# Kernel tuning notes

Hardware: AMD Instinct MI355X
Metric: run time of the kernel (lower is better)

## Reference

```python
import jax, jax.numpy as jnp
import numpy as np

B, T, D = 64, 2048, 256


def setup_inputs() -> dict:
    key = jax.random.key(0)
    k_x, k_len, k_w, k_b, k_a = jax.random.split(key, 5)
    xs = jax.random.normal(k_x, (B, T, D), dtype=jnp.float32)
    # ragged lengths -> prefix mask, mimicking per-sample slicing in the torch loop
    lens = jax.random.randint(k_len, (B,), T // 4, T + 1)
    mask = (jnp.arange(T)[None, :] < lens[:, None]).astype(jnp.int32)
    mask2 = jnp.ones((B, T), dtype=jnp.int32)  # unused by the module
    W = jax.random.normal(k_w, (D, D), dtype=jnp.float32) * (1.0 / np.sqrt(D))
    b = jax.random.normal(k_b, (D,), dtype=jnp.float32) * 0.01
    attn = jax.random.normal(k_a, (D,), dtype=jnp.float32)  # nn.Parameter(D,1) squeezed
    return {"xs": xs, "mask": mask, "mask2": mask2, "W": W, "b": b, "attn": attn}


def reference(xs, mask, mask2, W, b, attn):
    # h = tanh(Linear(x)); torch Linear: x @ W.T + b
    h = jnp.tanh(jnp.einsum("btd,ed->bte", xs, W) + b)          # [B,T,D]
    scores = jnp.einsum("btd,d->bt", h, attn)                    # [B,T]
    valid = mask.astype(bool)
    scores = jnp.where(valid, scores, -jnp.inf)                  # softmax over valid frames only
    w = jax.nn.softmax(scores, axis=1)[..., None]                # [B,T,1]
    mu = jnp.sum(xs * w, axis=1)                                 # [B,D]
    var = jnp.maximum(jnp.sum(xs * xs * w, axis=1) - mu * mu, 1e-5)
    return jnp.concatenate([mu, jnp.sqrt(var)], axis=1)          # [B,2D]
```

## Files before the change

kernel.cpp:

```cpp
#include <hip/hip_runtime.h>
#include <hip/hip_bf16.h>
#include <math.h>

#define PB 64
#define PT 2048
#define PD 256
#define PM (PB * PT)
#define SBM 64
#define NT (PM / SBM)
#define TPB (PT / SBM)

typedef __bf16 bf16x8 __attribute__((ext_vector_type(8)));
typedef short  s16x8  __attribute__((ext_vector_type(8)));
typedef float  f32x4  __attribute__((ext_vector_type(4)));

__device__ __forceinline__ short rne_bf16(float x) {
    unsigned u = __builtin_bit_cast(unsigned, x);
    return (short)((u + 0x7fffu + ((u >> 16) & 1u)) >> 16);
}

__device__ __forceinline__ void split_bf16(float x, short& hi, short& lo) {
    unsigned u = __builtin_bit_cast(unsigned, x);
    hi = (short)(u >> 16);
    float hf = __builtin_bit_cast(float, u & 0xffff0000u);
    lo = rne_bf16(x - hf);
}

__global__ __launch_bounds__(256) void prep_kernel(
    const float* __restrict__ W, short* __restrict__ Whi, short* __restrict__ Wlo)
{
    const int idx = blockIdx.x * 256 + threadIdx.x;
    const int e = idx >> 8;
    const int k = idx & 255;
    short h, l;
    split_bf16(W[idx], h, l);
    const int flat = (((e >> 4) * 8 + (k >> 5)) * 64 + ((k & 31) >> 3) * 16 + (e & 15)) * 8 + (k & 7);
    Whi[flat] = h;
    Wlo[flat] = l;
}

__global__ __launch_bounds__(256, 4) void score_kernel(
    const float* __restrict__ xs, const short* __restrict__ Whi,
    const short* __restrict__ Wlo, const float* __restrict__ bias,
    const float* __restrict__ attn, const int* __restrict__ mask,
    float* __restrict__ stats, float* __restrict__ part)
{
    __shared__ __align__(16) short Ah[4 * 8 * 64 * 8];
    __shared__ float sred[4][64];
    __shared__ float lw[64];

    const int tid  = threadIdx.x;
    const int tile = blockIdx.x;
    const int bm   = tile * SBM;

    const int mv = mask[bm + (tid & 63)];
    if (__ballot(mv != 0) == 0ull) {
        if (tid == 0) { stats[tile * 2] = -INFINITY; stats[tile * 2 + 1] = 0.f; }
        return;
    }

#pragma unroll
    for (int p = 0; p < 8; ++p) {
        const int r  = p * 8 + (tid >> 5);
        const int kb = tid & 31;
        const float4 a0 = *(const float4*)&xs[(bm + r) * PD + kb * 8];
        const float4 a1 = *(const float4*)&xs[(bm + r) * PD + kb * 8 + 4];
        const float f[8] = {a0.x, a0.y, a0.z, a0.w, a1.x, a1.y, a1.z, a1.w};
        s16x8 h;
#pragma unroll
        for (int j = 0; j < 8; ++j) h[j] = rne_bf16(f[j]);
        const int mt = r >> 4, m_loc = r & 15;
        const int kt = kb >> 2, quad = kb & 3;
        const int msw = m_loc ^ (kb & 7);
        *(s16x8*)&Ah[(((mt * 8 + kt) * 64) + quad * 16 + msw) * 8] = h;
    }
    __syncthreads();

    const int lane = tid & 63;
    const int w    = tid >> 6;
    const int quad = lane >> 4;
    const int nl   = lane & 15;

    f32x4 acc[4][4] = {};

#pragma unroll 2
    for (int kt = 0; kt < 8; ++kt) {
        bf16x8 bh[4], bl[4];
#pragma unroll
        for (int n = 0; n < 4; ++n) {
            const int nt = w * 4 + n;
            const int bidx = ((nt * 8 + kt) * 64 + lane) * 8;
            bh[n] = *(const bf16x8*)&Whi[bidx];
            bl[n] = *(const bf16x8*)&Wlo[bidx];
        }
        s16x8 ah[4];
        const int msw = nl ^ ((kt * 4 + quad) & 7);
#pragma unroll
        for (int m = 0; m < 4; ++m)
            ah[m] = *(const s16x8*)&Ah[((m * 8 + kt) * 64 + quad * 16 + msw) * 8];
#pragma unroll
        for (int m = 0; m < 4; ++m) {
            const bf16x8 ahm = __builtin_bit_cast(bf16x8, ah[m]);
#pragma unroll
            for (int n = 0; n < 4; ++n) {
                acc[m][n] = __builtin_amdgcn_mfma_f32_16x16x32_bf16(ahm, bh[n], acc[m][n], 0, 0, 0);
                acc[m][n] = __builtin_amdgcn_mfma_f32_16x16x32_bf16(ahm, bl[n], acc[m][n], 0, 0, 0);
            }
        }
    }

    float bv[4], av[4];
#pragma unroll
    for (int n = 0; n < 4; ++n) {
        const int col = w * 64 + n * 16 + nl;
        bv[n] = bias[col];
        av[n] = attn[col];
    }
#pragma unroll
    for (int m = 0; m < 4; ++m) {
        float rs[4] = {0.f, 0.f, 0.f, 0.f};
#pragma unroll
        for (int n = 0; n < 4; ++n) {
#pragma unroll
            for (int r = 0; r < 4; ++r) {
                const float u  = acc[m][n][r] + bv[n];
                const float e2 = __expf(2.f * u);
                const float th = 1.f - 2.f * __builtin_amdgcn_rcpf(e2 + 1.f);
                rs[r] = fmaf(th, av[n], rs[r]);
            }
        }
#pragma unroll
        for (int off = 1; off < 16; off <<= 1) {
#pragma unroll
            for (int r = 0; r < 4; ++r) rs[r] += __shfl_xor(rs[r], off);
        }
        if (nl == 0) {
#pragma unroll
            for (int r = 0; r < 4; ++r) sred[w][m * 16 + quad * 4 + r] = rs[r];
        }
    }
    __syncthreads();

    if (tid < 64) {
        float s = sred[0][tid] + sred[1][tid] + sred[2][tid] + sred[3][tid];
        const bool vld = (mv != 0);
        s = vld ? s : -INFINITY;
        float mx = s;
#pragma unroll
        for (int off = 1; off < 64; off <<= 1) mx = fmaxf(mx, __shfl_xor(mx, off));
        const float wt = vld ? __expf(s - mx) : 0.f;
        float zs = wt;
#pragma unroll
        for (int off = 1; off < 64; off <<= 1) zs += __shfl_xor(zs, off);
        lw[tid] = wt;
        if (tid == 0) { stats[tile * 2] = mx; stats[tile * 2 + 1] = zs; }
    }
    __syncthreads();

    float4* rmu = (float4*)Ah;
    float4* rm2 = rmu + 4 * 64;
    const int c  = tid & 63;
    const int tq = tid >> 6;
    float4 mu = {0.f, 0.f, 0.f, 0.f};
    float4 m2 = {0.f, 0.f, 0.f, 0.f};
#pragma unroll
    for (int i = 0; i < 16; ++i) {
        const int r  = tq * 16 + i;
        const float wv = lw[r];
        const float4 x = *(const float4*)&xs[(bm + r) * PD + c * 4];
        mu.x = fmaf(wv, x.x, mu.x); mu.y = fmaf(wv, x.y, mu.y);
        mu.z = fmaf(wv, x.z, mu.z); mu.w = fmaf(wv, x.w, mu.w);
        m2.x = fmaf(wv * x.x, x.x, m2.x); m2.y = fmaf(wv * x.y, x.y, m2.y);
        m2.z = fmaf(wv * x.z, x.z, m2.z); m2.w = fmaf(wv * x.w, x.w, m2.w);
    }
    rmu[tq * 64 + c] = mu;
    rm2[tq * 64 + c] = m2;
    __syncthreads();

    if (tid < 64) {
        float4 smu = rmu[tid], sm2 = rm2[tid];
#pragma unroll
        for (int q = 1; q < 4; ++q) {
            const float4 a = rmu[q * 64 + tid], d = rm2[q * 64 + tid];
            smu.x += a.x; smu.y += a.y; smu.z += a.z; smu.w += a.w;
            sm2.x += d.x; sm2.y += d.y; sm2.z += d.z; sm2.w += d.w;
        }
        const int base = tile * 512;
        *(float4*)&part[base + tid * 4]       = smu;
        *(float4*)&part[base + 256 + tid * 4] = sm2;
    }
}

__global__ __launch_bounds__(256) void finalize_kernel(
    const float* __restrict__ stats, const float* __restrict__ part,
    float* __restrict__ out)
{
    const int b = blockIdx.x;
    const int d = threadIdx.x;

    float M = -INFINITY;
#pragma unroll
    for (int t = 0; t < TPB; ++t) M = fmaxf(M, stats[(b * TPB + t) * 2]);

    float Z = 0.f, m1 = 0.f, m2 = 0.f;
#pragma unroll 4
    for (int t = 0; t < TPB; ++t) {
        const int g = b * TPB + t;
        const float zt = stats[g * 2 + 1];
        if (zt > 0.f) {
            const float f = __expf(stats[g * 2] - M);
            Z  = fmaf(zt, f, Z);
            m1 = fmaf(part[g * 512 + d],       f, m1);
            m2 = fmaf(part[g * 512 + 256 + d], f, m2);
        }
    }
    const float inv = 1.f / Z;
    m1 *= inv;
    m2 *= inv;
    const float var = fmaxf(m2 - m1 * m1, 1e-5f);
    out[b * 512 + d]       = m1;
    out[b * 512 + 256 + d] = sqrtf(var);
}

extern "C" void kernel_launch(void* const* d_in, const int* in_sizes, int n_in,
                              void* d_out, int out_size, void* d_ws, size_t ws_size,
                              hipStream_t stream) {
    const float* xs   = (const float*)d_in[0];
    const int*   mask = (const int*)d_in[1];
    const float* W    = (const float*)d_in[3];
    const float* bias = (const float*)d_in[4];
    const float* attn = (const float*)d_in[5];
    float* out = (float*)d_out;

    float* stats = (float*)d_ws;
    float* part  = stats + NT * 2;
    short* Whi   = (short*)(part + NT * 512);
    short* Wlo   = Whi + PD * PD;

    prep_kernel<<<PD * PD / 256, 256, 0, stream>>>(W, Whi, Wlo);
    score_kernel<<<NT, 256, 0, stream>>>(xs, Whi, Wlo, bias, attn, mask, stats, part);
    finalize_kernel<<<PB, 256, 0, stream>>>(stats, part, out);
}
```

Baseline: 229.2 us.

## Make score kernel persistent with W fragments held in registers across tiles

The score kernel becomes persistent: 256 blocks of 512 threads each process 8 tiles. Each wave loads its slice of the hi/lo bf16 W fragments into registers once and reuses them for every tile, instead of reloading W per k-step in every one of 2048 blocks. Tiles are interleaved so each block's tiles come from different batches, which spreads the work from masked-out tiles. The cost is heavy register pressure (32 bf16x8 vectors per thread), fewer blocks, and extra syncs inside the loop, which may limit latency hiding.

```diff
diff --git a/kernel.cpp b/kernel.cpp
--- a/kernel.cpp
+++ b/kernel.cpp
@@ -7,7 +7,7 @@
 #define PD 256
 #define PM (PB * PT)
 #define SBM 64
-#define NT (PM / SBM)
+#define NTILES (PM / SBM)
 #define TPB (PT / SBM)
 
 typedef __bf16 bf16x8 __attribute__((ext_vector_type(8)));
@@ -39,155 +39,162 @@
     Wlo[flat] = l;
 }
 
-__global__ __launch_bounds__(256, 4) void score_kernel(
+__global__ __launch_bounds__(512, 2) void score_kernel(
     const float* __restrict__ xs, const short* __restrict__ Whi,
     const short* __restrict__ Wlo, const float* __restrict__ bias,
     const float* __restrict__ attn, const int* __restrict__ mask,
     float* __restrict__ stats, float* __restrict__ part)
 {
     __shared__ __align__(16) short Ah[4 * 8 * 64 * 8];
-    __shared__ float sred[4][64];
+    __shared__ float sred[8][64];
     __shared__ float lw[64];
 
     const int tid  = threadIdx.x;
-    const int tile = blockIdx.x;
-    const int bm   = tile * SBM;
-
-    const int mv = mask[bm + (tid & 63)];
-    if (__ballot(mv != 0) == 0ull) {
-        if (tid == 0) { stats[tile * 2] = -INFINITY; stats[tile * 2 + 1] = 0.f; }
-        return;
-    }
-
-#pragma unroll
-    for (int p = 0; p < 8; ++p) {
-        const int r  = p * 8 + (tid >> 5);
-        const int kb = tid & 31;
-        const float4 a0 = *(const float4*)&xs[(bm + r) * PD + kb * 8];
-        const float4 a1 = *(const float4*)&xs[(bm + r) * PD + kb * 8 + 4];
-        const float f[8] = {a0.x, a0.y, a0.z, a0.w, a1.x, a1.y, a1.z, a1.w};
-        s16x8 h;
-#pragma unroll
-        for (int j = 0; j < 8; ++j) h[j] = rne_bf16(f[j]);
-        const int mt = r >> 4, m_loc = r & 15;
-        const int kt = kb >> 2, quad = kb & 3;
-        const int msw = m_loc ^ (kb & 7);
-        *(s16x8*)&Ah[(((mt * 8 + kt) * 64) + quad * 16 + msw) * 8] = h;
-    }
-    __syncthreads();
-
     const int lane = tid & 63;
     const int w    = tid >> 6;
     const int quad = lane >> 4;
     const int nl   = lane & 15;
-
-    f32x4 acc[4][4] = {};
-
-#pragma unroll 2
-    for (int kt = 0; kt < 8; ++kt) {
-        bf16x8 bh[4], bl[4];
-#pragma unroll
-        for (int n = 0; n < 4; ++n) {
-            const int nt = w * 4 + n;
+    const int blk  = blockIdx.x;
+
+    bf16x8 Bh[2][8], Bl[2][8];
+#pragma unroll
+    for (int n = 0; n < 2; ++n) {
+#pragma unroll
+        for (int kt = 0; kt < 8; ++kt) {
+            const int nt   = w * 2 + n;
             const int bidx = ((nt * 8 + kt) * 64 + lane) * 8;
-            bh[n] = *(const bf16x8*)&Whi[bidx];
-            bl[n] = *(const bf16x8*)&Wlo[bidx];
-        }
-        s16x8 ah[4];
-        const int msw = nl ^ ((kt * 4 + quad) & 7);
-#pragma unroll
-        for (int m = 0; m < 4; ++m)
-            ah[m] = *(const s16x8*)&Ah[((m * 8 + kt) * 64 + quad * 16 + msw) * 8];
-#pragma unroll
-        for (int m = 0; m < 4; ++m) {
-            const bf16x8 ahm = __builtin_bit_cast(bf16x8, ah[m]);
-#pragma unroll
-            for (int n = 0; n < 4; ++n) {
-                acc[m][n] = __builtin_amdgcn_mfma_f32_16x16x32_bf16(ahm, bh[n], acc[m][n], 0, 0, 0);
-                acc[m][n] = __builtin_amdgcn_mfma_f32_16x16x32_bf16(ahm, bl[n], acc[m][n], 0, 0, 0);
-            }
-        }
-    }
-
-    float bv[4], av[4];
-#pragma unroll
-    for (int n = 0; n < 4; ++n) {
-        const int col = w * 64 + n * 16 + nl;
+            Bh[n][kt] = *(const bf16x8*)&Whi[bidx];
+            Bl[n][kt] = *(const bf16x8*)&Wlo[bidx];
+        }
+    }
+    float bv[2], av[2];
+#pragma unroll
+    for (int n = 0; n < 2; ++n) {
+        const int col = w * 32 + n * 16 + nl;
         bv[n] = bias[col];
         av[n] = attn[col];
     }
-#pragma unroll
-    for (int m = 0; m < 4; ++m) {
-        float rs[4] = {0.f, 0.f, 0.f, 0.f};
-#pragma unroll
-        for (int n = 0; n < 4; ++n) {
-#pragma unroll
-            for (int r = 0; r < 4; ++r) {
-                const float u  = acc[m][n][r] + bv[n];
-                const float e2 = __expf(2.f * u);
-                const float th = 1.f - 2.f * __builtin_amdgcn_rcpf(e2 + 1.f);
-                rs[r] = fmaf(th, av[n], rs[r]);
-            }
-        }
-#pragma unroll
-        for (int off = 1; off < 16; off <<= 1) {
-#pragma unroll
-            for (int r = 0; r < 4; ++r) rs[r] += __shfl_xor(rs[r], off);
-        }
-        if (nl == 0) {
-#pragma unroll
-            for (int r = 0; r < 4; ++r) sred[w][m * 16 + quad * 4 + r] = rs[r];
-        }
-    }
-    __syncthreads();
-
-    if (tid < 64) {
-        float s = sred[0][tid] + sred[1][tid] + sred[2][tid] + sred[3][tid];
-        const bool vld = (mv != 0);
-        s = vld ? s : -INFINITY;
-        float mx = s;
-#pragma unroll
-        for (int off = 1; off < 64; off <<= 1) mx = fmaxf(mx, __shfl_xor(mx, off));
-        const float wt = vld ? __expf(s - mx) : 0.f;
-        float zs = wt;
-#pragma unroll
-        for (int off = 1; off < 64; off <<= 1) zs += __shfl_xor(zs, off);
-        lw[tid] = wt;
-        if (tid == 0) { stats[tile * 2] = mx; stats[tile * 2 + 1] = zs; }
-    }
-    __syncthreads();
-
-    float4* rmu = (float4*)Ah;
-    float4* rm2 = rmu + 4 * 64;
-    const int c  = tid & 63;
-    const int tq = tid >> 6;
-    float4 mu = {0.f, 0.f, 0.f, 0.f};
-    float4 m2 = {0.f, 0.f, 0.f, 0.f};
-#pragma unroll
-    for (int i = 0; i < 16; ++i) {
-        const int r  = tq * 16 + i;
-        const float wv = lw[r];
-        const float4 x = *(const float4*)&xs[(bm + r) * PD + c * 4];
-        mu.x = fmaf(wv, x.x, mu.x); mu.y = fmaf(wv, x.y, mu.y);
-        mu.z = fmaf(wv, x.z, mu.z); mu.w = fmaf(wv, x.w, mu.w);
-        m2.x = fmaf(wv * x.x, x.x, m2.x); m2.y = fmaf(wv * x.y, x.y, m2.y);
-        m2.z = fmaf(wv * x.z, x.z, m2.z); m2.w = fmaf(wv * x.w, x.w, m2.w);
-    }
-    rmu[tq * 64 + c] = mu;
-    rm2[tq * 64 + c] = m2;
-    __syncthreads();
-
-    if (tid < 64) {
-        float4 smu = rmu[tid], sm2 = rm2[tid];
-#pragma unroll
-        for (int q = 1; q < 4; ++q) {
-            const float4 a = rmu[q * 64 + tid], d = rm2[q * 64 + tid];
-            smu.x += a.x; smu.y += a.y; smu.z += a.z; smu.w += a.w;
-            sm2.x += d.x; sm2.y += d.y; sm2.z += d.z; sm2.w += d.w;
-        }
-        const int base = tile * 512;
-        *(float4*)&part[base + tid * 4]       = smu;
-        *(float4*)&part[base + 256 + tid * 4] = sm2;
+
+    for (int i = 0; i < 8; ++i) {
+        const int tile = (blk & 63) * 32 + i * 4 + (blk >> 6);
+        const int bm   = tile * SBM;
+
+        const int mv = mask[bm + lane];
+        if (__ballot(mv != 0) == 0ull) {
+            if (tid == 0) { stats[tile * 2] = -INFINITY; stats[tile * 2 + 1] = 0.f; }
+            continue;
+        }
+
+        __syncthreads();
+
+#pragma unroll
+        for (int p = 0; p < 4; ++p) {
+            const int r  = p * 16 + (tid >> 5);
+            const int kb = tid & 31;
+            const float4 a0 = *(const float4*)&xs[(bm + r) * PD + kb * 8];
+            const float4 a1 = *(const float4*)&xs[(bm + r) * PD + kb * 8 + 4];
+            const float f[8] = {a0.x, a0.y, a0.z, a0.w, a1.x, a1.y, a1.z, a1.w};
+            s16x8 h;
+#pragma unroll
+            for (int j = 0; j < 8; ++j) h[j] = rne_bf16(f[j]);
+            const int mt = r >> 4, m_loc = r & 15;
+            const int kt = kb >> 2, qd = kb & 3;
+            const int msw = m_loc ^ (kb & 7);
+            *(s16x8*)&Ah[(((mt * 8 + kt) * 64) + qd * 16 + msw) * 8] = h;
+        }
+        __syncthreads();
+
+        f32x4 acc[4][2] = {};
+#pragma unroll
+        for (int kt = 0; kt < 8; ++kt) {
+            s16x8 ah[4];
+            const int msw = nl ^ ((kt * 4 + quad) & 7);
+#pragma unroll
+            for (int m = 0; m < 4; ++m)
+                ah[m] = *(const s16x8*)&Ah[((m * 8 + kt) * 64 + quad * 16 + msw) * 8];
+#pragma unroll
+            for (int m = 0; m < 4; ++m) {
+                const bf16x8 ahm = __builtin_bit_cast(bf16x8, ah[m]);
+#pragma unroll
+                for (int n = 0; n < 2; ++n) {
+                    acc[m][n] = __builtin_amdgcn_mfma_f32_16x16x32_bf16(ahm, Bh[n][kt], acc[m][n], 0, 0, 0);
+                    acc[m][n] = __builtin_amdgcn_mfma_f32_16x16x32_bf16(ahm, Bl[n][kt], acc[m][n], 0, 0, 0);
+                }
+            }
+        }
+
+#pragma unroll
+        for (int m = 0; m < 4; ++m) {
+            float rs[4] = {0.f, 0.f, 0.f, 0.f};
+#pragma unroll
+            for (int n = 0; n < 2; ++n) {
+#pragma unroll
+                for (int r = 0; r < 4; ++r) {
+                    const float u  = acc[m][n][r] + bv[n];
+                    const float e2 = __expf(2.f * u);
+                    const float th = 1.f - 2.f * __builtin_amdgcn_rcpf(e2 + 1.f);
+                    rs[r] = fmaf(th, av[n], rs[r]);
+                }
+            }
+#pragma unroll
+            for (int off = 1; off < 16; off <<= 1) {
+#pragma unroll
+                for (int r = 0; r < 4; ++r) rs[r] += __shfl_xor(rs[r], off);
+            }
+            if (nl == 0) {
+#pragma unroll
+                for (int r = 0; r < 4; ++r) sred[w][m * 16 + quad * 4 + r] = rs[r];
+            }
+        }
+        __syncthreads();
+
+        if (tid < 64) {
+            float s = sred[0][tid] + sred[1][tid] + sred[2][tid] + sred[3][tid]
+                    + sred[4][tid] + sred[5][tid] + sred[6][tid] + sred[7][tid];
+            const bool vld = (mv != 0);
+            s = vld ? s : -INFINITY;
+            float mx = s;
+#pragma unroll
+            for (int off = 1; off < 64; off <<= 1) mx = fmaxf(mx, __shfl_xor(mx, off));
+            const float wt = vld ? __expf(s - mx) : 0.f;
+            float zs = wt;
+#pragma unroll
+            for (int off = 1; off < 64; off <<= 1) zs += __shfl_xor(zs, off);
+            lw[tid] = wt;
+            if (tid == 0) { stats[tile * 2] = mx; stats[tile * 2 + 1] = zs; }
+        }
+        __syncthreads();
+
+        float4* rmu = (float4*)Ah;
+        float4* rm2 = rmu + 8 * 64;
+        float4 mu = {0.f, 0.f, 0.f, 0.f};
+        float4 m2 = {0.f, 0.f, 0.f, 0.f};
+#pragma unroll
+        for (int j = 0; j < 8; ++j) {
+            const int r  = w * 8 + j;
+            const float wv = lw[r];
+            const float4 x = *(const float4*)&xs[(bm + r) * PD + lane * 4];
+            mu.x = fmaf(wv, x.x, mu.x); mu.y = fmaf(wv, x.y, mu.y);
+            mu.z = fmaf(wv, x.z, mu.z); mu.w = fmaf(wv, x.w, mu.w);
+            m2.x = fmaf(wv * x.x, x.x, m2.x); m2.y = fmaf(wv * x.y, x.y, m2.y);
+            m2.z = fmaf(wv * x.z, x.z, m2.z); m2.w = fmaf(wv * x.w, x.w, m2.w);
+        }
+        rmu[w * 64 + lane] = mu;
+        rm2[w * 64 + lane] = m2;
+        __syncthreads();
+
+        if (tid < 64) {
+            float4 smu = rmu[tid], sm2 = rm2[tid];
+#pragma unroll
+            for (int q = 1; q < 8; ++q) {
+                const float4 a = rmu[q * 64 + tid], d = rm2[q * 64 + tid];
+                smu.x += a.x; smu.y += a.y; smu.z += a.z; smu.w += a.w;
+                sm2.x += d.x; sm2.y += d.y; sm2.z += d.z; sm2.w += d.w;
+            }
+            const int base = tile * 512;
+            *(float4*)&part[base + tid * 4]       = smu;
+            *(float4*)&part[base + 256 + tid * 4] = sm2;
+        }
     }
 }
 
@@ -233,11 +240,11 @@
     float* out = (float*)d_out;
 
     float* stats = (float*)d_ws;
-    float* part  = stats + NT * 2;
-    short* Whi   = (short*)(part + NT * 512);
+    float* part  = stats + NTILES * 2;
+    short* Whi   = (short*)(part + NTILES * 512);
     short* Wlo   = Whi + PD * PD;
 
     prep_kernel<<<PD * PD / 256, 256, 0, stream>>>(W, Whi, Wlo);
-    score_kernel<<<NT, 256, 0, stream>>>(xs, Whi, Wlo, bias, attn, mask, stats, part);
+    score_kernel<<<256, 512, 0, stream>>>(xs, Whi, Wlo, bias, attn, mask, stats, part);
     finalize_kernel<<<PB, 256, 0, stream>>>(stats, part, out);
 }
```

Result: slower. 242.0 us (+5.6%).

## Load A fragments directly from global, drop LDS staging and a barrier

Applied to the files above, without the earlier changes.

The score kernel no longer stages the bf16-converted x tile in shared memory. Each wave now reads its MFMA A fragments straight from global memory inside the k-loop and converts them with packed v_cvt_pk_bf16_f32. The softmax reduction now runs redundantly in every wave, and the weights are broadcast with __shfl instead of through LDS, which removes a __syncthreads and the lw buffer. The cost is that all four waves re-read the same x rows from global/L2 (four times the A traffic), and conversion now uses hardware rounding instead of the explicit RNE routine.

```diff
diff --git a/kernel.cpp b/kernel.cpp
--- a/kernel.cpp
+++ b/kernel.cpp
@@ -7,7 +7,7 @@
 #define PD 256
 #define PM (PB * PT)
 #define SBM 64
-#define NT (PM / SBM)
+#define NTILES (PM / SBM)
 #define TPB (PT / SBM)
 
 typedef __bf16 bf16x8 __attribute__((ext_vector_type(8)));
@@ -24,6 +24,12 @@
     hi = (short)(u >> 16);
     float hf = __builtin_bit_cast(float, u & 0xffff0000u);
     lo = rne_bf16(x - hf);
+}
+
+__device__ __forceinline__ int cvt_pk_bf16(float a, float b) {
+    int r;
+    asm("v_cvt_pk_bf16_f32 %0, %1, %2" : "=v"(r) : "v"(a), "v"(b));
+    return r;
 }
 
 __global__ __launch_bounds__(256) void prep_kernel(
@@ -45,62 +51,48 @@
     const float* __restrict__ attn, const int* __restrict__ mask,
     float* __restrict__ stats, float* __restrict__ part)
 {
-    __shared__ __align__(16) short Ah[4 * 8 * 64 * 8];
     __shared__ float sred[4][64];
-    __shared__ float lw[64];
+    __shared__ __align__(16) float4 rmu[4 * 64];
+    __shared__ __align__(16) float4 rm2[4 * 64];
 
     const int tid  = threadIdx.x;
-    const int tile = blockIdx.x;
-    const int bm   = tile * SBM;
-
-    const int mv = mask[bm + (tid & 63)];
-    if (__ballot(mv != 0) == 0ull) {
-        if (tid == 0) { stats[tile * 2] = -INFINITY; stats[tile * 2 + 1] = 0.f; }
-        return;
-    }
-
-#pragma unroll
-    for (int p = 0; p < 8; ++p) {
-        const int r  = p * 8 + (tid >> 5);
-        const int kb = tid & 31;
-        const float4 a0 = *(const float4*)&xs[(bm + r) * PD + kb * 8];
-        const float4 a1 = *(const float4*)&xs[(bm + r) * PD + kb * 8 + 4];
-        const float f[8] = {a0.x, a0.y, a0.z, a0.w, a1.x, a1.y, a1.z, a1.w};
-        s16x8 h;
-#pragma unroll
-        for (int j = 0; j < 8; ++j) h[j] = rne_bf16(f[j]);
-        const int mt = r >> 4, m_loc = r & 15;
-        const int kt = kb >> 2, quad = kb & 3;
-        const int msw = m_loc ^ (kb & 7);
-        *(s16x8*)&Ah[(((mt * 8 + kt) * 64) + quad * 16 + msw) * 8] = h;
-    }
-    __syncthreads();
-
     const int lane = tid & 63;
     const int w    = tid >> 6;
     const int quad = lane >> 4;
     const int nl   = lane & 15;
+    const int tile = blockIdx.x;
+    const int bm   = tile * SBM;
+
+    const int mv = mask[bm + lane];
+    if (__ballot(mv != 0) == 0ull) {
+        if (tid == 0) { stats[tile * 2] = -INFINITY; stats[tile * 2 + 1] = 0.f; }
+        return;
+    }
+
+    const float* xrow0 = xs + (bm + nl) * PD + quad * 8;
 
     f32x4 acc[4][4] = {};
-
 #pragma unroll 2
     for (int kt = 0; kt < 8; ++kt) {
         bf16x8 bh[4], bl[4];
 #pragma unroll
         for (int n = 0; n < 4; ++n) {
-            const int nt = w * 4 + n;
+            const int nt   = w * 4 + n;
             const int bidx = ((nt * 8 + kt) * 64 + lane) * 8;
             bh[n] = *(const bf16x8*)&Whi[bidx];
             bl[n] = *(const bf16x8*)&Wlo[bidx];
         }
-        s16x8 ah[4];
-        const int msw = nl ^ ((kt * 4 + quad) & 7);
-#pragma unroll
-        for (int m = 0; m < 4; ++m)
-            ah[m] = *(const s16x8*)&Ah[((m * 8 + kt) * 64 + quad * 16 + msw) * 8];
 #pragma unroll
         for (int m = 0; m < 4; ++m) {
-            const bf16x8 ahm = __builtin_bit_cast(bf16x8, ah[m]);
+            const float* xr = xrow0 + m * 16 * PD + kt * 32;
+            const float4 a0 = *(const float4*)xr;
+            const float4 a1 = *(const float4*)(xr + 4);
+            int4 pk;
+            pk.x = cvt_pk_bf16(a0.x, a0.y);
+            pk.y = cvt_pk_bf16(a0.z, a0.w);
+            pk.z = cvt_pk_bf16(a1.x, a1.y);
+            pk.w = cvt_pk_bf16(a1.z, a1.w);
+            const bf16x8 ahm = __builtin_bit_cast(bf16x8, pk);
 #pragma unroll
             for (int n = 0; n < 4; ++n) {
                 acc[m][n] = __builtin_amdgcn_mfma_f32_16x16x32_bf16(ahm, bh[n], acc[m][n], 0, 0, 0);
@@ -141,40 +133,32 @@
     }
     __syncthreads();
 
-    if (tid < 64) {
-        float s = sred[0][tid] + sred[1][tid] + sred[2][tid] + sred[3][tid];
-        const bool vld = (mv != 0);
-        s = vld ? s : -INFINITY;
-        float mx = s;
-#pragma unroll
-        for (int off = 1; off < 64; off <<= 1) mx = fmaxf(mx, __shfl_xor(mx, off));
-        const float wt = vld ? __expf(s - mx) : 0.f;
-        float zs = wt;
-#pragma unroll
-        for (int off = 1; off < 64; off <<= 1) zs += __shfl_xor(zs, off);
-        lw[tid] = wt;
-        if (tid == 0) { stats[tile * 2] = mx; stats[tile * 2 + 1] = zs; }
-    }
-    __syncthreads();
-
-    float4* rmu = (float4*)Ah;
-    float4* rm2 = rmu + 4 * 64;
-    const int c  = tid & 63;
-    const int tq = tid >> 6;
+    float s = sred[0][lane] + sred[1][lane] + sred[2][lane] + sred[3][lane];
+    const bool vld = (mv != 0);
+    s = vld ? s : -INFINITY;
+    float mx = s;
+#pragma unroll
+    for (int off = 1; off < 64; off <<= 1) mx = fmaxf(mx, __shfl_xor(mx, off));
+    const float wt = vld ? __expf(s - mx) : 0.f;
+    float zs = wt;
+#pragma unroll
+    for (int off = 1; off < 64; off <<= 1) zs += __shfl_xor(zs, off);
+    if (tid == 0) { stats[tile * 2] = mx; stats[tile * 2 + 1] = zs; }
+
     float4 mu = {0.f, 0.f, 0.f, 0.f};
     float4 m2 = {0.f, 0.f, 0.f, 0.f};
 #pragma unroll
-    for (int i = 0; i < 16; ++i) {
-        const int r  = tq * 16 + i;
-        const float wv = lw[r];
-        const float4 x = *(const float4*)&xs[(bm + r) * PD + c * 4];
+    for (int j = 0; j < 16; ++j) {
+        const int r  = w * 16 + j;
+        const float wv = __shfl(wt, r);
+        const float4 x = *(const float4*)&xs[(bm + r) * PD + lane * 4];
         mu.x = fmaf(wv, x.x, mu.x); mu.y = fmaf(wv, x.y, mu.y);
         mu.z = fmaf(wv, x.z, mu.z); mu.w = fmaf(wv, x.w, mu.w);
         m2.x = fmaf(wv * x.x, x.x, m2.x); m2.y = fmaf(wv * x.y, x.y, m2.y);
         m2.z = fmaf(wv * x.z, x.z, m2.z); m2.w = fmaf(wv * x.w, x.w, m2.w);
     }
-    rmu[tq * 64 + c] = mu;
-    rm2[tq * 64 + c] = m2;
+    rmu[w * 64 + lane] = mu;
+    rm2[w * 64 + lane] = m2;
     __syncthreads();
 
     if (tid < 64) {
@@ -233,11 +217,11 @@
     float* out = (float*)d_out;
 
     float* stats = (float*)d_ws;
-    float* part  = stats + NT * 2;
-    short* Whi   = (short*)(part + NT * 512);
+    float* part  = stats + NTILES * 2;
+    short* Whi   = (short*)(part + NTILES * 512);
     short* Wlo   = Whi + PD * PD;
 
     prep_kernel<<<PD * PD / 256, 256, 0, stream>>>(W, Whi, Wlo);
-    score_kernel<<<NT, 256, 0, stream>>>(xs, Whi, Wlo, bias, attn, mask, stats, part);
+    score_kernel<<<NTILES, 256, 0, stream>>>(xs, Whi, Wlo, bias, attn, mask, stats, part);
     finalize_kernel<<<PB, 256, 0, stream>>>(stats, part, out);
 }
```

Result: slower. 324.8 us (+41.7%).
